# Kernel tuning notes

Hardware: AMD Instinct MI355X
Metric: run time of the kernel (lower is better)

The kernel has to match this reference:

```python
import jax, jax.numpy as jnp
import numpy as np
import math

N_HEADS = 16

def setup_inputs() -> dict:
    key = jax.random.key(0)
    k1, k2, k3 = jax.random.split(key, 3)
    B, S, D = 2, 2048, 1024
    x = jax.random.normal(k1, (B, S, D), dtype=jnp.float32)
    qkv = 0.01 * jax.random.normal(k2, (3 * D, D), dtype=jnp.float32)
    wo = 0.01 * jax.random.normal(k3, (D, D), dtype=jnp.float32)
    return {"x": x, "qkv": qkv, "wo": wo}

def reference(x, qkv, wo):
    B, S, D = x.shape
    H = N_HEADS
    dh = D // H
    QKV = x @ qkv.T                      # [B,S,3D]
    Q, K, V = jnp.split(QKV, 3, axis=-1)
    q = Q.reshape(B, S, H, dh).transpose(0, 2, 1, 3)  # [B,H,S,dh]
    k = K.reshape(B, S, H, dh).transpose(0, 2, 1, 3)
    v = V.reshape(B, S, H, dh).transpose(0, 2, 1, 3)
    scores = jnp.einsum('bhqd,bhkd->bhqk', q, k) / math.sqrt(float(dh))
    # Faithful to original: multiply by lower-triangular mask, then set
    # exact zeros to -inf (masked positions become 0 then -inf).
    mask = jnp.tril(jnp.ones((S, S), dtype=scores.dtype))
    scores = scores * mask[None, None, :, :]
    scores = jnp.where(scores == 0, -jnp.inf, scores)
    attn = jax.nn.softmax(scores, axis=-1)
    out = jnp.einsum('bhqk,bhkd->bhqd', attn, v)       # [B,H,S,dh]
    out = out.transpose(0, 2, 1, 3).reshape(B, S, D)
    return out @ wo.T
```

## Files before the change

kernel.cpp:

```cpp
#include <hip/hip_runtime.h>

typedef unsigned short u16;
typedef unsigned int u32;
typedef __bf16 bf16x8 __attribute__((ext_vector_type(8)));
typedef float f32x4 __attribute__((ext_vector_type(4)));
typedef u16 u16x4 __attribute__((ext_vector_type(4)));

#define GL2LDS16(g, l)                                                         \
    __builtin_amdgcn_global_load_lds(                                          \
        (__attribute__((address_space(1))) const void*)(g),                    \
        (__attribute__((address_space(3))) void*)(l), 16, 0, 0)

#define SYNC_VM(n) asm volatile("s_waitcnt vmcnt(" #n ")\ns_barrier" ::: "memory")
#define BAR()      asm volatile("s_barrier" ::: "memory")

__device__ __forceinline__ u16 f2bf(float f) {
    union { float f; u32 u; } x; x.f = f;
    u32 r = x.u + 0x7FFFu + ((x.u >> 16) & 1u);
    return (u16)(r >> 16);
}

__device__ __forceinline__ u32 pack2bf(float f0, float f1) {
    union { float f; u32 u; } a, b;
    a.f = f0; b.f = f1;
    return __builtin_amdgcn_perm(b.u + 0x8000u, a.u + 0x8000u, 0x07060302u);
}

__device__ __forceinline__ float bits2f(u32 u) {
    union { u32 u; float f; } x; x.u = u; return x.f;
}

__device__ __forceinline__ bf16x8 scale_frag(bf16x8 v) {
#pragma unroll
    for (int i = 0; i < 8; ++i) v[i] = (__bf16)((float)v[i] * 0.1803368801f);
    return v;
}

__global__ __launch_bounds__(256) void convert_all_kernel(const float* __restrict__ x,
                                                          const float* __restrict__ qkv,
                                                          const float* __restrict__ wo,
                                                          u16* __restrict__ out) {
    int i = (blockIdx.x * 256 + threadIdx.x) * 4;
    const float* src;
    int off;
    if (i < 4194304)      { src = x;   off = i; }
    else if (i < 7340032) { src = qkv; off = i - 4194304; }
    else                  { src = wo;  off = i - 7340032; }
    float4 v = *(const float4*)(src + off);
    u16x4 o;
    o.x = f2bf(v.x); o.y = f2bf(v.y); o.z = f2bf(v.z); o.w = f2bf(v.w);
    *(u16x4*)(out + i) = o;
}

template <int TM, bool OUT_BF16>
__global__ __launch_bounds__(256) void gemm_bt(const u16* __restrict__ A,
                                               const u16* __restrict__ B,
                                               void* __restrict__ Cout,
                                               int M, int N, int K) {
    constexpr int MI = TM / 32;
    __shared__ u16 As[2][TM * 32];
    __shared__ u16 Bs[2][128 * 32];
    const int tid = threadIdx.x;
    const int w = tid >> 6, lane = tid & 63, ln = lane & 15, qd = lane >> 4;
    const int wr = w >> 1, wc = w & 1;
    const int m0 = blockIdx.y * TM, n0 = blockIdx.x * 128;

    const int srow = tid >> 2, scol = (tid & 3) * 8;
    const u16* Abase = A + (size_t)(m0 + srow) * K + scol;
    const u16* Bbase = B + (size_t)(n0 + srow) * K + scol;

    f32x4 acc[MI][4] = {};
    const int nsteps = K >> 5;

#pragma unroll
    for (int it = 0; it < TM / 64; ++it)
        GL2LDS16(Abase + (size_t)(it * 64) * K, &As[0][(tid + it * 256) * 8]);
#pragma unroll
    for (int it = 0; it < 2; ++it)
        GL2LDS16(Bbase + (size_t)(it * 64) * K, &Bs[0][(tid + it * 256) * 8]);

    for (int s = 0; s < nsteps; ++s) {
        const u16* Ab = As[s & 1];
        const u16* Bb = Bs[s & 1];
        if (s + 1 < nsteps) {
            const int nk = (s + 1) << 5;
            const int nb = (s + 1) & 1;
#pragma unroll
            for (int it = 0; it < TM / 64; ++it)
                GL2LDS16(Abase + (size_t)(it * 64) * K + nk, &As[nb][(tid + it * 256) * 8]);
#pragma unroll
            for (int it = 0; it < 2; ++it)
                GL2LDS16(Bbase + (size_t)(it * 64) * K + nk, &Bs[nb][(tid + it * 256) * 8]);
            if constexpr (TM == 128) SYNC_VM(4); else SYNC_VM(3);
        } else {
            SYNC_VM(0);
        }

        bf16x8 af[MI], bfr[4];
#pragma unroll
        for (int i = 0; i < MI; ++i)
            af[i] = *(const bf16x8*)&Ab[(wr * (TM / 2) + i * 16 + ln) * 32 + qd * 8];
#pragma unroll
        for (int j = 0; j < 4; ++j)
            bfr[j] = *(const bf16x8*)&Bb[(wc * 64 + j * 16 + ln) * 32 + qd * 8];
#pragma unroll
        for (int i = 0; i < MI; ++i)
#pragma unroll
            for (int j = 0; j < 4; ++j)
                acc[i][j] = __builtin_amdgcn_mfma_f32_16x16x32_bf16(af[i], bfr[j], acc[i][j], 0, 0, 0);
        BAR();
    }

#pragma unroll
    for (int i = 0; i < MI; ++i)
#pragma unroll
        for (int j = 0; j < 4; ++j)
#pragma unroll
            for (int r = 0; r < 4; ++r) {
                int row = m0 + wr * (TM / 2) + i * 16 + qd * 4 + r;
                int col = n0 + wc * 64 + j * 16 + ln;
                float v = acc[i][j][r];
                if constexpr (OUT_BF16)
                    ((u16*)Cout)[(size_t)row * N + col] = f2bf(v);
                else
                    ((float*)Cout)[(size_t)row * N + col] = v;
            }
}

__global__ __launch_bounds__(256) void vtrans_kernel(const u16* __restrict__ QKV,
                                                     u16* __restrict__ VtG) {
    __shared__ u16 T[64 * 72];
    const int tid = threadIdx.x;
    const int bh = blockIdx.y;
    const int b = bh >> 4, h = bh & 15;
    const int s0 = blockIdx.x * 64;
#pragma unroll
    for (int it = 0; it < 2; ++it) {
        int idx = it * 256 + tid;
        int sl = idx >> 3, dg = (idx & 7) << 3;
        union { uint4 v; u16 u[8]; } raw;
        raw.v = *(const uint4*)(QKV + (size_t)(b * 2048 + s0 + sl) * 3072 + 2048 + h * 64 + dg);
#pragma unroll
        for (int j = 0; j < 8; ++j) T[(dg + j) * 72 + sl] = raw.u[j];
    }
    __syncthreads();
#pragma unroll
    for (int it = 0; it < 2; ++it) {
        int idx = it * 256 + tid;
        int d = idx >> 3, sg = (idx & 7) << 3;
        *(uint4*)(VtG + ((size_t)(bh * 64 + d)) * 2048 + s0 + sg) = *(uint4*)&T[d * 72 + sg];
    }
}

__global__ __launch_bounds__(256) void attn_kernel(u16* __restrict__ QKV,
                                                   const u16* __restrict__ VtG,
                                                   u16* __restrict__ AO,
                                                   float* __restrict__ Lp) {
    __shared__ u16 Ks[2][64 * 64];
    __shared__ u16 Vts[2][64 * 64];
    __shared__ u16 Pls[4][16 * 64];

    const int tid = threadIdx.x;
    const int w = tid >> 6, lane = tid & 63, ln = lane & 15, qd = lane >> 4;
    const int b = blockIdx.z, h = blockIdx.y;
    const int pair = blockIdx.x >> 1;
    const int k = blockIdx.x & 1;
    const int qtA = pair, qtB = 31 - pair;
    const int XA = qtA * 64 + w * 16, XB = qtB * 64 + w * 16;
    const int myqA = XA + ln, myqB = XB + ln;
    const int bh = b * 16 + h;
    const int swz = ln & 7;
    const int nch = qtB + 1;

    const int sr0 = tid >> 3;
    const int sg = (tid & 7) ^ (sr0 & 7);
    const u16* ksrc = QKV + (size_t)(b * 2048 + sr0) * 3072 + 1024 + h * 64 + sg * 8;
    const u16* vsrc = VtG + (size_t)(bh * 64 + sr0) * 2048 + sg * 8;

    GL2LDS16(ksrc + (size_t)(k * 64) * 3072, &Ks[0][tid * 8]);
    GL2LDS16(ksrc + (size_t)(k * 64 + 32) * 3072, &Ks[0][tid * 8 + 2048]);
    GL2LDS16(vsrc + k * 64, &Vts[0][tid * 8]);
    GL2LDS16(vsrc + k * 64 + 32 * 2048, &Vts[0][tid * 8 + 2048]);

    const u16* qpA = QKV + (size_t)(b * 2048 + myqA) * 3072 + h * 64;
    const u16* qpB = QKV + (size_t)(b * 2048 + myqB) * 3072 + h * 64;
    bf16x8 qfA0 = scale_frag(*(const bf16x8*)(qpA + qd * 8));
    bf16x8 qfA1 = scale_frag(*(const bf16x8*)(qpA + 32 + qd * 8));
    bf16x8 qfB0 = scale_frag(*(const bf16x8*)(qpB + qd * 8));
    bf16x8 qfB1 = scale_frag(*(const bf16x8*)(qpB + 32 + qd * 8));

    f32x4 oA[4] = {}, oB[4] = {};
    float lA = 0.f, lB = 0.f;
    u16* Pw = Pls[w];

    for (int c = k; c < nch; c += 2) {
        const int j = (c - k) >> 1;
        const int buf = j & 1;
        if (c + 2 < nch) {
            const int k1 = (c + 2) * 64;
            const int nb = buf ^ 1;
            GL2LDS16(ksrc + (size_t)k1 * 3072, &Ks[nb][tid * 8]);
            GL2LDS16(ksrc + (size_t)(k1 + 32) * 3072, &Ks[nb][tid * 8 + 2048]);
            GL2LDS16(vsrc + k1, &Vts[nb][tid * 8]);
            GL2LDS16(vsrc + k1 + 32 * 2048, &Vts[nb][tid * 8 + 2048]);
            SYNC_VM(4);
        } else {
            SYNC_VM(0);
        }
        const u16* Kb = Ks[buf];
        const u16* Vb = Vts[buf];
        const bool actA = (c * 64 <= XA + 15);

        f32x4 sA[4], sB[4];
#pragma unroll
        for (int kt = 0; kt < 4; ++kt) {
            const u16* kr = Kb + (kt * 16 + ln) * 64;
            bf16x8 kf0 = *(const bf16x8*)(kr + ((qd ^ swz) * 8));
            bf16x8 kf1 = *(const bf16x8*)(kr + (((qd + 4) ^ swz) * 8));
            f32x4 z = {0.f, 0.f, 0.f, 0.f};
            z = __builtin_amdgcn_mfma_f32_16x16x32_bf16(kf0, qfB0, z, 0, 0, 0);
            z = __builtin_amdgcn_mfma_f32_16x16x32_bf16(kf1, qfB1, z, 0, 0, 0);
            sB[kt] = z;
            if (actA) {
                f32x4 y = {0.f, 0.f, 0.f, 0.f};
                y = __builtin_amdgcn_mfma_f32_16x16x32_bf16(kf0, qfA0, y, 0, 0, 0);
                y = __builtin_amdgcn_mfma_f32_16x16x32_bf16(kf1, qfA1, y, 0, 0, 0);
                sA[kt] = y;
            }
        }

        if (c * 64 + 63 > XB) {
#pragma unroll
            for (int kt = 0; kt < 4; ++kt)
#pragma unroll
                for (int r = 0; r < 4; ++r) {
                    int key = c * 64 + kt * 16 + qd * 4 + r;
                    if (key > myqB) sB[kt][r] = -1e30f;
                }
        }
#pragma unroll
        for (int kt = 0; kt < 4; ++kt) {
            float p0 = exp2f(sB[kt][0]), p1 = exp2f(sB[kt][1]);
            float p2 = exp2f(sB[kt][2]), p3 = exp2f(sB[kt][3]);
            lB += (p0 + p1) + (p2 + p3);
            uint2 pk = {pack2bf(p0, p1), pack2bf(p2, p3)};
            int g = kt * 2 + (qd >> 1);
            *(uint2*)&Pw[ln * 64 + ((g ^ swz) * 8) + (qd & 1) * 4] = pk;
        }
        bf16x8 pfB0 = *(const bf16x8*)&Pw[ln * 64 + ((qd ^ swz) * 8)];
        bf16x8 pfB1 = *(const bf16x8*)&Pw[ln * 64 + (((qd + 4) ^ swz) * 8)];

        bf16x8 pfA0, pfA1;
        if (actA) {
            if (c * 64 + 63 > XA) {
#pragma unroll
                for (int kt = 0; kt < 4; ++kt)
#pragma unroll
                    for (int r = 0; r < 4; ++r) {
                        int key = c * 64 + kt * 16 + qd * 4 + r;
                        if (key > myqA) sA[kt][r] = -1e30f;
                    }
            }
#pragma unroll
            for (int kt = 0; kt < 4; ++kt) {
                float p0 = exp2f(sA[kt][0]), p1 = exp2f(sA[kt][1]);
                float p2 = exp2f(sA[kt][2]), p3 = exp2f(sA[kt][3]);
                lA += (p0 + p1) + (p2 + p3);
                uint2 pk = {pack2bf(p0, p1), pack2bf(p2, p3)};
                int g = kt * 2 + (qd >> 1);
                *(uint2*)&Pw[ln * 64 + ((g ^ swz) * 8) + (qd & 1) * 4] = pk;
            }
            pfA0 = *(const bf16x8*)&Pw[ln * 64 + ((qd ^ swz) * 8)];
            pfA1 = *(const bf16x8*)&Pw[ln * 64 + (((qd + 4) ^ swz) * 8)];
        }

#pragma unroll
        for (int dt = 0; dt < 4; ++dt) {
            const u16* vr = Vb + (dt * 16 + ln) * 64;
            bf16x8 vf0 = *(const bf16x8*)(vr + ((qd ^ swz) * 8));
            bf16x8 vf1 = *(const bf16x8*)(vr + (((qd + 4) ^ swz) * 8));
            oB[dt] = __builtin_amdgcn_mfma_f32_16x16x32_bf16(vf0, pfB0, oB[dt], 0, 0, 0);
            oB[dt] = __builtin_amdgcn_mfma_f32_16x16x32_bf16(vf1, pfB1, oB[dt], 0, 0, 0);
            if (actA) {
                oA[dt] = __builtin_amdgcn_mfma_f32_16x16x32_bf16(vf0, pfA0, oA[dt], 0, 0, 0);
                oA[dt] = __builtin_amdgcn_mfma_f32_16x16x32_bf16(vf1, pfA1, oA[dt], 0, 0, 0);
            }
        }
        BAR();
    }

    lA += __shfl_xor(lA, 16); lA += __shfl_xor(lA, 32);
    lB += __shfl_xor(lB, 16); lB += __shfl_xor(lB, 32);
    u16* Op = k ? (QKV + 2048) : AO;
    const size_t ost = k ? 3072 : 1024;
    if (qd == 0) {
        Lp[(size_t)k * 65536 + (size_t)(b * 2048 + myqA) * 16 + h] = lA;
        Lp[(size_t)k * 65536 + (size_t)(b * 2048 + myqB) * 16 + h] = lB;
    }
#pragma unroll
    for (int dt = 0; dt < 4; ++dt) {
        uint2 ovA = {pack2bf(oA[dt][0], oA[dt][1]), pack2bf(oA[dt][2], oA[dt][3])};
        *(uint2*)&Op[(size_t)(b * 2048 + myqA) * ost + h * 64 + dt * 16 + qd * 4] = ovA;
        uint2 ovB = {pack2bf(oB[dt][0], oB[dt][1]), pack2bf(oB[dt][2], oB[dt][3])};
        *(uint2*)&Op[(size_t)(b * 2048 + myqB) * ost + h * 64 + dt * 16 + qd * 4] = ovB;
    }
}

__global__ __launch_bounds__(256) void normalize_kernel(u16* __restrict__ AO,
                                                        const u16* __restrict__ QKV,
                                                        const float* __restrict__ Lp) {
    int g = blockIdx.x * 256 + threadIdx.x;
    int row = g >> 7;
    int col = (g & 127) << 3;
    int h = col >> 6;
    float l = Lp[(size_t)row * 16 + h] + Lp[65536 + (size_t)row * 16 + h];
    float inv = 1.0f / l;
    u16* pa = AO + (size_t)row * 1024 + col;
    const u16* pb = QKV + (size_t)row * 3072 + 2048 + col;
    uint4 va = *(uint4*)pa;
    uint4 vb = *(const uint4*)pb;
    const u32* a = (const u32*)&va;
    const u32* bb = (const u32*)&vb;
    u32 res[4];
#pragma unroll
    for (int i = 0; i < 4; ++i) {
        float a0 = bits2f(a[i] << 16), a1 = bits2f(a[i] & 0xFFFF0000u);
        float b0 = bits2f(bb[i] << 16), b1 = bits2f(bb[i] & 0xFFFF0000u);
        res[i] = pack2bf((a0 + b0) * inv, (a1 + b1) * inv);
    }
    *(uint4*)pa = *(uint4*)&res[0];
}

extern "C" void kernel_launch(void* const* d_in, const int* in_sizes, int n_in,
                              void* d_out, int out_size, void* d_ws, size_t ws_size,
                              hipStream_t stream) {
    const float* x   = (const float*)d_in[0];
    const float* qkv = (const float*)d_in[1];
    const float* wo  = (const float*)d_in[2];
    float* out = (float*)d_out;

    char* ws = (char*)d_ws;
    u16* xb    = (u16*)(ws + 0);
    u16* qkvb  = (u16*)(ws + 8388608);
    float* Lp  = (float*)(ws + 8388608);
    u16* wob   = (u16*)(ws + 14680064);
    u16* QKVo  = (u16*)(ws + 16777216);
    u16* AO    = (u16*)(ws + 41943040);
    u16* VtG   = (u16*)(ws + 0);

    convert_all_kernel<<<8192, 256, 0, stream>>>(x, qkv, wo, xb);

    gemm_bt<128, true><<<dim3(24, 32), 256, 0, stream>>>(xb, qkvb, QKVo, 4096, 3072, 1024);

    vtrans_kernel<<<dim3(32, 32), 256, 0, stream>>>(QKVo, VtG);

    attn_kernel<<<dim3(32, 16, 2), 256, 0, stream>>>(QKVo, VtG, AO, Lp);

    normalize_kernel<<<2048, 256, 0, stream>>>(AO, QKVo, Lp);

    gemm_bt<64, false><<<dim3(8, 64), 256, 0, stream>>>(AO, wob, out, 4096, 1024, 1024);
}
```

Baseline: 203.3 us.

## Fuse V transpose into QKV GEMM and restructure attention per-wave query tiles

The QKV GEMM epilogue now writes the V columns transposed straight into a VtG buffer, which removes the separate vtrans kernel and the V columns of QKV are no longer stored. The attention kernel is reorganised so each wave owns a 64-query tile (four 16-row subtiles) and reuses the K fragments from LDS across all four. V fragments are loaded directly from global memory instead of being staged in LDS, and the grid is halved. The intent is to raise MFMA reuse per K/V load and cut a launch plus a transpose pass. The risks are more register pressure from the 4x4 output accumulators, uncoalesced global V loads, and load imbalance because waves in a block cover different causal lengths.

```diff
diff --git a/kernel.cpp b/kernel.cpp
--- a/kernel.cpp
+++ b/kernel.cpp
@@ -52,10 +52,11 @@
     *(u16x4*)(out + i) = o;
 }
 
-template <int TM, bool OUT_BF16>
+template <int TM, bool OUT_BF16, bool FUSE_VT>
 __global__ __launch_bounds__(256) void gemm_bt(const u16* __restrict__ A,
                                                const u16* __restrict__ B,
                                                void* __restrict__ Cout,
+                                               u16* __restrict__ VtG,
                                                int M, int N, int K) {
     constexpr int MI = TM / 32;
     __shared__ u16 As[2][TM * 32];
@@ -111,6 +112,23 @@
         BAR();
     }
 
+    if (FUSE_VT && n0 >= 2048) {
+        const int bq = m0 >> 11;
+        const int sl = (m0 & 2047) + wr * (TM / 2) + qd * 4;
+#pragma unroll
+        for (int i = 0; i < MI; ++i)
+#pragma unroll
+            for (int j = 0; j < 4; ++j) {
+                int d = n0 - 2048 + wc * 64 + j * 16 + ln;
+                int vrow = (bq * 16 + (d >> 6)) * 64 + (d & 63);
+                u16x4 ov;
+                ov.x = f2bf(acc[i][j][0]); ov.y = f2bf(acc[i][j][1]);
+                ov.z = f2bf(acc[i][j][2]); ov.w = f2bf(acc[i][j][3]);
+                *(u16x4*)&VtG[(size_t)vrow * 2048 + sl + i * 16] = ov;
+            }
+        return;
+    }
+
 #pragma unroll
     for (int i = 0; i < MI; ++i)
 #pragma unroll
@@ -127,182 +145,129 @@
             }
 }
 
-__global__ __launch_bounds__(256) void vtrans_kernel(const u16* __restrict__ QKV,
-                                                     u16* __restrict__ VtG) {
-    __shared__ u16 T[64 * 72];
-    const int tid = threadIdx.x;
-    const int bh = blockIdx.y;
-    const int b = bh >> 4, h = bh & 15;
-    const int s0 = blockIdx.x * 64;
-#pragma unroll
-    for (int it = 0; it < 2; ++it) {
-        int idx = it * 256 + tid;
-        int sl = idx >> 3, dg = (idx & 7) << 3;
-        union { uint4 v; u16 u[8]; } raw;
-        raw.v = *(const uint4*)(QKV + (size_t)(b * 2048 + s0 + sl) * 3072 + 2048 + h * 64 + dg);
-#pragma unroll
-        for (int j = 0; j < 8; ++j) T[(dg + j) * 72 + sl] = raw.u[j];
-    }
-    __syncthreads();
-#pragma unroll
-    for (int it = 0; it < 2; ++it) {
-        int idx = it * 256 + tid;
-        int d = idx >> 3, sg = (idx & 7) << 3;
-        *(uint4*)(VtG + ((size_t)(bh * 64 + d)) * 2048 + s0 + sg) = *(uint4*)&T[d * 72 + sg];
-    }
-}
-
 __global__ __launch_bounds__(256) void attn_kernel(u16* __restrict__ QKV,
                                                    const u16* __restrict__ VtG,
                                                    u16* __restrict__ AO,
                                                    float* __restrict__ Lp) {
     __shared__ u16 Ks[2][64 * 64];
-    __shared__ u16 Vts[2][64 * 64];
     __shared__ u16 Pls[4][16 * 64];
 
     const int tid = threadIdx.x;
     const int w = tid >> 6, lane = tid & 63, ln = lane & 15, qd = lane >> 4;
     const int b = blockIdx.z, h = blockIdx.y;
-    const int pair = blockIdx.x >> 1;
+    const int g = 7 - (blockIdx.x >> 1);
     const int k = blockIdx.x & 1;
-    const int qtA = pair, qtB = 31 - pair;
-    const int XA = qtA * 64 + w * 16, XB = qtB * 64 + w * 16;
-    const int myqA = XA + ln, myqB = XB + ln;
+    const int Bw = 4 * g + w;
+    const int q0 = Bw * 64;
     const int bh = b * 16 + h;
     const int swz = ln & 7;
-    const int nch = qtB + 1;
+    const int cMax = 4 * g + 3;
 
     const int sr0 = tid >> 3;
     const int sg = (tid & 7) ^ (sr0 & 7);
     const u16* ksrc = QKV + (size_t)(b * 2048 + sr0) * 3072 + 1024 + h * 64 + sg * 8;
-    const u16* vsrc = VtG + (size_t)(bh * 64 + sr0) * 2048 + sg * 8;
-
     GL2LDS16(ksrc + (size_t)(k * 64) * 3072, &Ks[0][tid * 8]);
     GL2LDS16(ksrc + (size_t)(k * 64 + 32) * 3072, &Ks[0][tid * 8 + 2048]);
-    GL2LDS16(vsrc + k * 64, &Vts[0][tid * 8]);
-    GL2LDS16(vsrc + k * 64 + 32 * 2048, &Vts[0][tid * 8 + 2048]);
-
-    const u16* qpA = QKV + (size_t)(b * 2048 + myqA) * 3072 + h * 64;
-    const u16* qpB = QKV + (size_t)(b * 2048 + myqB) * 3072 + h * 64;
-    bf16x8 qfA0 = scale_frag(*(const bf16x8*)(qpA + qd * 8));
-    bf16x8 qfA1 = scale_frag(*(const bf16x8*)(qpA + 32 + qd * 8));
-    bf16x8 qfB0 = scale_frag(*(const bf16x8*)(qpB + qd * 8));
-    bf16x8 qfB1 = scale_frag(*(const bf16x8*)(qpB + 32 + qd * 8));
-
-    f32x4 oA[4] = {}, oB[4] = {};
-    float lA = 0.f, lB = 0.f;
+
+    bf16x8 qf[4][2];
+#pragma unroll
+    for (int i = 0; i < 4; ++i) {
+        const u16* qp = QKV + (size_t)(b * 2048 + q0 + i * 16 + ln) * 3072 + h * 64;
+        qf[i][0] = scale_frag(*(const bf16x8*)(qp + qd * 8));
+        qf[i][1] = scale_frag(*(const bf16x8*)(qp + 32 + qd * 8));
+    }
+
+    const u16* vbase = VtG + (size_t)(bh * 64) * 2048;
+    f32x4 o[4][4] = {};
+    float l[4] = {};
     u16* Pw = Pls[w];
 
-    for (int c = k; c < nch; c += 2) {
-        const int j = (c - k) >> 1;
-        const int buf = j & 1;
-        if (c + 2 < nch) {
-            const int k1 = (c + 2) * 64;
-            const int nb = buf ^ 1;
-            GL2LDS16(ksrc + (size_t)k1 * 3072, &Ks[nb][tid * 8]);
-            GL2LDS16(ksrc + (size_t)(k1 + 32) * 3072, &Ks[nb][tid * 8 + 2048]);
-            GL2LDS16(vsrc + k1, &Vts[nb][tid * 8]);
-            GL2LDS16(vsrc + k1 + 32 * 2048, &Vts[nb][tid * 8 + 2048]);
-            SYNC_VM(4);
+    for (int c = k; c <= cMax; c += 2) {
+        const int buf = ((c - k) >> 1) & 1;
+        if (c + 2 <= cMax) {
+            GL2LDS16(ksrc + (size_t)((c + 2) * 64) * 3072, &Ks[buf ^ 1][tid * 8]);
+            GL2LDS16(ksrc + (size_t)((c + 2) * 64 + 32) * 3072, &Ks[buf ^ 1][tid * 8 + 2048]);
+            SYNC_VM(2);
         } else {
             SYNC_VM(0);
         }
-        const u16* Kb = Ks[buf];
-        const u16* Vb = Vts[buf];
-        const bool actA = (c * 64 <= XA + 15);
-
-        f32x4 sA[4], sB[4];
-#pragma unroll
-        for (int kt = 0; kt < 4; ++kt) {
-            const u16* kr = Kb + (kt * 16 + ln) * 64;
-            bf16x8 kf0 = *(const bf16x8*)(kr + ((qd ^ swz) * 8));
-            bf16x8 kf1 = *(const bf16x8*)(kr + (((qd + 4) ^ swz) * 8));
-            f32x4 z = {0.f, 0.f, 0.f, 0.f};
-            z = __builtin_amdgcn_mfma_f32_16x16x32_bf16(kf0, qfB0, z, 0, 0, 0);
-            z = __builtin_amdgcn_mfma_f32_16x16x32_bf16(kf1, qfB1, z, 0, 0, 0);
-            sB[kt] = z;
-            if (actA) {
-                f32x4 y = {0.f, 0.f, 0.f, 0.f};
-                y = __builtin_amdgcn_mfma_f32_16x16x32_bf16(kf0, qfA0, y, 0, 0, 0);
-                y = __builtin_amdgcn_mfma_f32_16x16x32_bf16(kf1, qfA1, y, 0, 0, 0);
-                sA[kt] = y;
-            }
-        }
-
-        if (c * 64 + 63 > XB) {
-#pragma unroll
-            for (int kt = 0; kt < 4; ++kt)
-#pragma unroll
-                for (int r = 0; r < 4; ++r) {
-                    int key = c * 64 + kt * 16 + qd * 4 + r;
-                    if (key > myqB) sB[kt][r] = -1e30f;
+
+        if (c <= Bw) {
+            const u16* Kb = Ks[buf];
+            bf16x8 vf[4][2];
+#pragma unroll
+            for (int dt = 0; dt < 4; ++dt) {
+                const u16* vr = vbase + (size_t)(dt * 16 + ln) * 2048 + c * 64;
+                vf[dt][0] = *(const bf16x8*)(vr + qd * 8);
+                vf[dt][1] = *(const bf16x8*)(vr + 32 + qd * 8);
+            }
+            bf16x8 kf[4][2];
+#pragma unroll
+            for (int kt = 0; kt < 4; ++kt) {
+                const u16* kr = Kb + (kt * 16 + ln) * 64;
+                kf[kt][0] = *(const bf16x8*)(kr + ((qd ^ swz) * 8));
+                kf[kt][1] = *(const bf16x8*)(kr + (((qd + 4) ^ swz) * 8));
+            }
+
+            bf16x8 pf[4][2];
+#pragma unroll
+            for (int i = 0; i < 4; ++i) {
+                f32x4 s[4];
+#pragma unroll
+                for (int kt = 0; kt < 4; ++kt) {
+                    f32x4 z = {0.f, 0.f, 0.f, 0.f};
+                    z = __builtin_amdgcn_mfma_f32_16x16x32_bf16(kf[kt][0], qf[i][0], z, 0, 0, 0);
+                    z = __builtin_amdgcn_mfma_f32_16x16x32_bf16(kf[kt][1], qf[i][1], z, 0, 0, 0);
+                    s[kt] = z;
+                }
+                if (c == Bw) {
+                    int myq = q0 + i * 16 + ln;
+#pragma unroll
+                    for (int kt = 0; kt < 4; ++kt)
+#pragma unroll
+                        for (int r = 0; r < 4; ++r) {
+                            int key = c * 64 + kt * 16 + qd * 4 + r;
+                            if (key > myq) s[kt][r] = -1e30f;
+                        }
+                }
+#pragma unroll
+                for (int kt = 0; kt < 4; ++kt) {
+                    float p0 = exp2f(s[kt][0]), p1 = exp2f(s[kt][1]);
+                    float p2 = exp2f(s[kt][2]), p3 = exp2f(s[kt][3]);
+                    l[i] += (p0 + p1) + (p2 + p3);
+                    uint2 pk = {pack2bf(p0, p1), pack2bf(p2, p3)};
+                    int gg = kt * 2 + (qd >> 1);
+                    *(uint2*)&Pw[ln * 64 + ((gg ^ swz) * 8) + (qd & 1) * 4] = pk;
+                }
+                pf[i][0] = *(const bf16x8*)&Pw[ln * 64 + ((qd ^ swz) * 8)];
+                pf[i][1] = *(const bf16x8*)&Pw[ln * 64 + (((qd + 4) ^ swz) * 8)];
+            }
+
+#pragma unroll
+            for (int dt = 0; dt < 4; ++dt)
+#pragma unroll
+                for (int i = 0; i < 4; ++i) {
+                    o[i][dt] = __builtin_amdgcn_mfma_f32_16x16x32_bf16(vf[dt][0], pf[i][0], o[i][dt], 0, 0, 0);
+                    o[i][dt] = __builtin_amdgcn_mfma_f32_16x16x32_bf16(vf[dt][1], pf[i][1], o[i][dt], 0, 0, 0);
                 }
         }
-#pragma unroll
-        for (int kt = 0; kt < 4; ++kt) {
-            float p0 = exp2f(sB[kt][0]), p1 = exp2f(sB[kt][1]);
-            float p2 = exp2f(sB[kt][2]), p3 = exp2f(sB[kt][3]);
-            lB += (p0 + p1) + (p2 + p3);
-            uint2 pk = {pack2bf(p0, p1), pack2bf(p2, p3)};
-            int g = kt * 2 + (qd >> 1);
-            *(uint2*)&Pw[ln * 64 + ((g ^ swz) * 8) + (qd & 1) * 4] = pk;
-        }
-        bf16x8 pfB0 = *(const bf16x8*)&Pw[ln * 64 + ((qd ^ swz) * 8)];
-        bf16x8 pfB1 = *(const bf16x8*)&Pw[ln * 64 + (((qd + 4) ^ swz) * 8)];
-
-        bf16x8 pfA0, pfA1;
-        if (actA) {
-            if (c * 64 + 63 > XA) {
-#pragma unroll
-                for (int kt = 0; kt < 4; ++kt)
-#pragma unroll
-                    for (int r = 0; r < 4; ++r) {
-                        int key = c * 64 + kt * 16 + qd * 4 + r;
-                        if (key > myqA) sA[kt][r] = -1e30f;
-                    }
-            }
-#pragma unroll
-            for (int kt = 0; kt < 4; ++kt) {
-                float p0 = exp2f(sA[kt][0]), p1 = exp2f(sA[kt][1]);
-                float p2 = exp2f(sA[kt][2]), p3 = exp2f(sA[kt][3]);
-                lA += (p0 + p1) + (p2 + p3);
-                uint2 pk = {pack2bf(p0, p1), pack2bf(p2, p3)};
-                int g = kt * 2 + (qd >> 1);
-                *(uint2*)&Pw[ln * 64 + ((g ^ swz) * 8) + (qd & 1) * 4] = pk;
-            }
-            pfA0 = *(const bf16x8*)&Pw[ln * 64 + ((qd ^ swz) * 8)];
-            pfA1 = *(const bf16x8*)&Pw[ln * 64 + (((qd + 4) ^ swz) * 8)];
-        }
-
-#pragma unroll
-        for (int dt = 0; dt < 4; ++dt) {
-            const u16* vr = Vb + (dt * 16 + ln) * 64;
-            bf16x8 vf0 = *(const bf16x8*)(vr + ((qd ^ swz) * 8));
-            bf16x8 vf1 = *(const bf16x8*)(vr + (((qd + 4) ^ swz) * 8));
-            oB[dt] = __builtin_amdgcn_mfma_f32_16x16x32_bf16(vf0, pfB0, oB[dt], 0, 0, 0);
-            oB[dt] = __builtin_amdgcn_mfma_f32_16x16x32_bf16(vf1, pfB1, oB[dt], 0, 0, 0);
-            if (actA) {
-                oA[dt] = __builtin_amdgcn_mfma_f32_16x16x32_bf16(vf0, pfA0, oA[dt], 0, 0, 0);
-                oA[dt] = __builtin_amdgcn_mfma_f32_16x16x32_bf16(vf1, pfA1, oA[dt], 0, 0, 0);
-            }
-        }
         BAR();
     }
 
-    lA += __shfl_xor(lA, 16); lA += __shfl_xor(lA, 32);
-    lB += __shfl_xor(lB, 16); lB += __shfl_xor(lB, 32);
     u16* Op = k ? (QKV + 2048) : AO;
     const size_t ost = k ? 3072 : 1024;
-    if (qd == 0) {
-        Lp[(size_t)k * 65536 + (size_t)(b * 2048 + myqA) * 16 + h] = lA;
-        Lp[(size_t)k * 65536 + (size_t)(b * 2048 + myqB) * 16 + h] = lB;
-    }
-#pragma unroll
-    for (int dt = 0; dt < 4; ++dt) {
-        uint2 ovA = {pack2bf(oA[dt][0], oA[dt][1]), pack2bf(oA[dt][2], oA[dt][3])};
-        *(uint2*)&Op[(size_t)(b * 2048 + myqA) * ost + h * 64 + dt * 16 + qd * 4] = ovA;
-        uint2 ovB = {pack2bf(oB[dt][0], oB[dt][1]), pack2bf(oB[dt][2], oB[dt][3])};
-        *(uint2*)&Op[(size_t)(b * 2048 + myqB) * ost + h * 64 + dt * 16 + qd * 4] = ovB;
+#pragma unroll
+    for (int i = 0; i < 4; ++i) {
+        float li = l[i];
+        li += __shfl_xor(li, 16); li += __shfl_xor(li, 32);
+        int myq = q0 + i * 16 + ln;
+        if (qd == 0)
+            Lp[(size_t)k * 65536 + (size_t)(b * 2048 + myq) * 16 + h] = li;
+#pragma unroll
+        for (int dt = 0; dt < 4; ++dt) {
+            uint2 ov = {pack2bf(o[i][dt][0], o[i][dt][1]), pack2bf(o[i][dt][2], o[i][dt][3])};
+            *(uint2*)&Op[(size_t)(b * 2048 + myq) * ost + h * 64 + dt * 16 + qd * 4] = ov;
+        }
     }
 }
 
@@ -346,17 +311,17 @@
     u16* wob   = (u16*)(ws + 14680064);
     u16* QKVo  = (u16*)(ws + 16777216);
     u16* AO    = (u16*)(ws + 41943040);
-    u16* VtG   = (u16*)(ws + 0);
+    u16* VtG   = (u16*)(ws + 50331648);
 
     convert_all_kernel<<<8192, 256, 0, stream>>>(x, qkv, wo, xb);
 
-    gemm_bt<128, true><<<dim3(24, 32), 256, 0, stream>>>(xb, qkvb, QKVo, 4096, 3072, 1024);
-
-    vtrans_kernel<<<dim3(32, 32), 256, 0, stream>>>(QKVo, VtG);
-
-    attn_kernel<<<dim3(32, 16, 2), 256, 0, stream>>>(QKVo, VtG, AO, Lp);
+    gemm_bt<128, true, true><<<dim3(24, 32), 256, 0, stream>>>(xb, qkvb, QKVo, VtG,
+                                                               4096, 3072, 1024);
+
+    attn_kernel<<<dim3(16, 16, 2), 256, 0, stream>>>(QKVo, VtG, AO, Lp);
 
     normalize_kernel<<<2048, 256, 0, stream>>>(AO, QKVo, Lp);
 
-    gemm_bt<64, false><<<dim3(8, 64), 256, 0, stream>>>(AO, wob, out, 4096, 1024, 1024);
-}
+    gemm_bt<64, false, false><<<dim3(8, 64), 256, 0, stream>>>(AO, wob, out, nullptr,
+                                                               4096, 1024, 1024);
+}
```

New measurement: 231.2 us. +13.8%, slower.
